# Optimization experiments

Hardware: AMD Instinct MI355X
Metric: run time of the kernel (lower is better)

The kernel has to match this reference:

```python
import math
import jax, jax.numpy as jnp
import numpy as np

N_ANGLES = 180  # len(thetas), thetas = k*pi/180 for k in 0..179
IMG_SIZE = 256
BATCH = 2


def setup_inputs() -> dict:
    key = jax.random.key(0)
    image = jax.random.normal(key, (BATCH, 1, IMG_SIZE, IMG_SIZE), dtype=jnp.float32)
    return {"image": image}


def _bilinear_gather(flat_img, yi, xi, S, dtype):
    # flat_img: (B, S*S); yi, xi: (A, S, S) int32 corner indices
    valid = (xi >= 0) & (xi < S) & (yi >= 0) & (yi < S)
    idx = jnp.clip(yi, 0, S - 1) * S + jnp.clip(xi, 0, S - 1)
    v = jnp.take(flat_img, idx.reshape(-1), axis=1).reshape((flat_img.shape[0],) + idx.shape)
    return v * valid.astype(dtype)  # zeros padding_mode


def reference(image):
    # Radon.forward with circle=False: pad image to diagonal size, rotate
    # sampling grid per angle, grid_sample (bilinear, align_corners=True,
    # padding_mode='zeros'), sum over rows -> sinogram (B, 1, S, n_angles).
    B, _, S0, _ = image.shape
    S = int(math.ceil(math.sqrt(2.0) * S0))  # padded size (363 for 256)
    pad_total = S - S0
    pb, pa = pad_total // 2, pad_total - pad_total // 2
    img = jnp.pad(image[:, 0], ((0, 0), (pb, pa), (pb, pa)))  # (B, S, S)

    thetas = jnp.arange(N_ANGLES, dtype=jnp.float32) * jnp.float32(np.pi / N_ANGLES)
    cos = jnp.cos(thetas)[:, None, None]  # (A,1,1)
    sin = jnp.sin(thetas)[:, None, None]

    # affine_grid(align_corners=True) base grid in [-1, 1]
    lin = jnp.linspace(-1.0, 1.0, S, dtype=jnp.float32)
    x = lin[None, None, :]  # width coord
    y = lin[None, :, None]  # height coord
    gx = cos * x + sin * y   # (A, S, S) sample x
    gy = -sin * x + cos * y  # (A, S, S) sample y

    # grid_sample align_corners=True pixel coordinates
    ix = (gx + 1.0) * 0.5 * (S - 1)
    iy = (gy + 1.0) * 0.5 * (S - 1)
    x0 = jnp.floor(ix)
    y0 = jnp.floor(iy)
    wx = ix - x0
    wy = iy - y0
    x0i = x0.astype(jnp.int32)
    y0i = y0.astype(jnp.int32)

    flat = img.reshape(B, S * S)
    dt = img.dtype
    v00 = _bilinear_gather(flat, y0i, x0i, S, dt)
    v01 = _bilinear_gather(flat, y0i, x0i + 1, S, dt)
    v10 = _bilinear_gather(flat, y0i + 1, x0i, S, dt)
    v11 = _bilinear_gather(flat, y0i + 1, x0i + 1, S, dt)

    samp = (v00 * (1 - wx) * (1 - wy) + v01 * wx * (1 - wy)
            + v10 * (1 - wx) * wy + v11 * wx * wy)  # (B, A, S, S)

    sino = samp.sum(axis=2)             # sum over rows -> (B, A, S)
    return sino.transpose(0, 2, 1)[:, None]  # (B, 1, S, A)
```

## Files before the change

kernel.cpp:

```cpp
#include <hip/hip_runtime.h>

#define N_ANGLES 180
#define IMG 256
#define SPAD 363
#define PB 53
#define BATCH 2
#define TOTAL (BATCH * N_ANGLES * SPAD)
#define RSPLIT 4

#define QB 6
#define QDIM (IMG + 2 * QB)
#define QELEMS (QDIM * QDIM)
#define NTAB (2 * BATCH)
#define COFF ((QB - PB) * (QDIM + 1))

__global__ __launch_bounds__(256) void prep_quad(const float* __restrict__ img,
                                                 float4* __restrict__ quad) {
    const int e = blockIdx.x * 256 + threadIdx.x;
    if (e >= NTAB * QELEMS) return;
    const int xq = e % QDIM;
    const int t2 = e / QDIM;
    const int yq = t2 % QDIM;
    const int tb = t2 / QDIM;
    const int b  = tb & (BATCH - 1);
    const int v  = tb >> 1;
    const int x = xq - QB, y = yq - QB;
    const float* ib = img + b * (IMG * IMG);
    auto val = [&](int yy, int xx) -> float {
        if ((unsigned)yy >= (unsigned)IMG || (unsigned)xx >= (unsigned)IMG) return 0.0f;
        return v ? ib[xx * IMG + yy]
                 : ib[yy * IMG + xx];
    };
    float4 q;
    q.x = val(y, x);     q.y = val(y, x + 1);
    q.z = val(y + 1, x); q.w = val(y + 1, x + 1);
    quad[e] = q;
}

__global__ __launch_bounds__(256) void radon_quad(const float4* __restrict__ quad,
                                                  float* __restrict__ out) {
    const int gid = blockIdx.x * 256 + threadIdx.x;
    const int o = gid >> 2;
    const int p = gid & 3;
    if (o >= TOTAL) return;

    const int t  = o % SPAD;
    const int ba = o / SPAD;
    const int a  = ba % N_ANGLES;
    const int b  = ba / N_ANGLES;

    const float theta = (float)a * 0.017453292519943295f;
    float s, c;
    sincosf(theta, &s, &c);

    const float d  = 2.0f / 362.0f;
    const float lt = fmaf((float)t, d, -1.0f);
    const float ct  = c * lt;
    const float mst = -s * lt;

    const bool useT = (s > fabsf(c));
    const float sA = useT ? c   : s;
    const float cA = useT ? mst : ct;
    const float sB = useT ? s   : c;
    const float cB = useT ? ct  : mst;
    const float4* __restrict__ qt = quad + ((useT ? BATCH : 0) + b) * QELEMS;

    const float fA = sA * 181.0f, gA = (cA + 1.0f) * 181.0f;
    const float fB = sB * 181.0f, gB = (cB + 1.0f) * 181.0f;
    const float v0A = fmaf(fA, -1.0f, gA), dvA = fA * d * 181.0f;
    const float v0B = fmaf(fB, -1.0f, gB), dvB = fB * d * 181.0f;
    const float stepA = fA * d;
    const float stepB = fB * d;

    float rlo = 0.0f, rhi = 362.0f;
    {
        const float lo = 51.0f, hi = 310.0f;
        if (fabsf(stepA) < 1e-5f) {
            if (v0A < lo || v0A > hi) { rlo = 363.0f; rhi = -1.0f; }
        } else {
            const float r0 = (lo - v0A) / stepA;
            const float r1 = (hi - v0A) / stepA;
            rlo = fmaxf(rlo, fminf(r0, r1));
            rhi = fminf(rhi, fmaxf(r0, r1));
        }
        if (fabsf(stepB) < 1e-5f) {
            if (v0B < lo || v0B > hi) { rlo = 363.0f; rhi = -1.0f; }
        } else {
            const float r0 = (lo - v0B) / stepB;
            const float r1 = (hi - v0B) / stepB;
            rlo = fmaxf(rlo, fminf(r0, r1));
            rhi = fminf(rhi, fmaxf(r0, r1));
        }
    }
    const int rmin = max(0,   (int)floorf(rlo));
    const int rmax = min(362, (int)ceilf(rhi));

    float acc = 0.0f;
#pragma unroll 2
    for (int r = rmin + ((p - rmin) & 3); r <= rmax; r += RSPLIT) {
        const float rf = (float)r;
        const float ix = fmaf(rf, stepA, v0A);
        const float iy = fmaf(rf, stepB, v0B);
        const float wx = ix - floorf(ix);
        const float wy = iy - floorf(iy);
        const int   xi = (int)ix;
        const int   yi = (int)iy;
        const float4 q = qt[yi * QDIM + xi + COFF];
        const float omwx = 1.0f - wx;
        const float omwy = 1.0f - wy;
        const float top = fmaf(q.y, wx, q.x * omwx);
        const float bot = fmaf(q.w, wx, q.z * omwx);
        acc = fmaf(bot, wy, fmaf(top, omwy, acc));
    }

    acc += __shfl_xor(acc, 1);
    acc += __shfl_xor(acc, 2);

    if (p == 0) {
        out[(b * SPAD + t) * N_ANGLES + a] = acc;
    }
}


__global__ __launch_bounds__(256) void transpose_kernel(const float* __restrict__ img,
                                                        float* __restrict__ imgT) {
    __shared__ float tile[32][33];
    const int b  = blockIdx.z;
    const int tx = blockIdx.x * 32;
    const int ty = blockIdx.y * 32;
    const int lx = threadIdx.x & 31;
    const int l8 = threadIdx.x >> 5;
    const float* ib = img  + b * IMG * IMG;
    float*       ob = imgT + b * IMG * IMG;
#pragma unroll
    for (int i = 0; i < 4; ++i) {
        const int ly = l8 + i * 8;
        tile[ly][lx] = ib[(ty + ly) * IMG + tx + lx];
    }
    __syncthreads();
#pragma unroll
    for (int i = 0; i < 4; ++i) {
        const int ly = l8 + i * 8;
        ob[(tx + ly) * IMG + ty + lx] = tile[lx][ly];
    }
}

#define SAMPLE(r, CHECKED)                                                     \
    {                                                                          \
        const float lr  = fmaf((float)(r), d, -1.0f);                          \
        const float ix  = fmaf(fA, lr, gA);                                    \
        const float iy  = fmaf(fB, lr, gB);                                    \
        const float wx  = ix - floorf(ix);                                     \
        const float wy  = iy - floorf(iy);                                     \
        const int   xi  = (int)ix;                                             \
        const int   yi  = (int)iy;                                             \
        float v00, v01, v10, v11;                                              \
        if (CHECKED) {                                                         \
            const int xA = xi - PB, yA = yi - PB;                              \
            const bool vx0 = (unsigned)xA       < (unsigned)IMG;               \
            const bool vx1 = (unsigned)(xA + 1) < (unsigned)IMG;               \
            const bool vy0 = (unsigned)yA       < (unsigned)IMG;               \
            const bool vy1 = (unsigned)(yA + 1) < (unsigned)IMG;               \
            const float* rp = base + yA * IMG + xA;                            \
            v00 = (vx0 && vy0) ? rp[0]       : 0.0f;                           \
            v01 = (vx1 && vy0) ? rp[1]       : 0.0f;                           \
            v10 = (vx0 && vy1) ? rp[IMG]     : 0.0f;                           \
            v11 = (vx1 && vy1) ? rp[IMG + 1] : 0.0f;                           \
        } else {                                                               \
            const float* rp = base + (yi * IMG + xi - (PB * IMG + PB));        \
            v00 = rp[0]; v01 = rp[1]; v10 = rp[IMG]; v11 = rp[IMG + 1];        \
        }                                                                      \
        const float omwx = 1.0f - wx;                                          \
        const float omwy = 1.0f - wy;                                          \
        const float top  = fmaf(v01, wx, v00 * omwx);                          \
        const float bot  = fmaf(v11, wx, v10 * omwx);                          \
        acc = fmaf(bot, wy, fmaf(top, omwy, acc));                             \
    }

template <bool HAVE_T>
__global__ __launch_bounds__(256) void radon_kernel(const float* __restrict__ img,
                                                    const float* __restrict__ imgT,
                                                    float* __restrict__ out) {
    const int gid = blockIdx.x * 256 + threadIdx.x;
    const int o = gid >> 1;
    const int p = gid & 1;
    if (o >= TOTAL) return;

    const int t  = o % SPAD;
    const int ba = o / SPAD;
    const int a  = ba % N_ANGLES;
    const int b  = ba / N_ANGLES;

    const float theta = (float)a * 0.017453292519943295f;
    float s, c;
    sincosf(theta, &s, &c);

    const float d  = 2.0f / 362.0f;
    const float lt = fmaf((float)t, d, -1.0f);
    const float ct  = c * lt;
    const float mst = -s * lt;

    const bool useT = HAVE_T && (s > fabsf(c));
    const float sA = useT ? c   : s;
    const float cA = useT ? mst : ct;
    const float sB = useT ? s   : c;
    const float cB = useT ? ct  : mst;
    const float* __restrict__ base = (useT ? imgT : img) + b * (IMG * IMG);

    const float fA = sA * 181.0f;
    const float gA = (cA + 1.0f) * 181.0f;
    const float fB = sB * 181.0f;
    const float gB = (cB + 1.0f) * 181.0f;

    const float v0A = fmaf(fA, -1.0f, gA), dvA = fA * d;
    const float v0B = fmaf(fB, -1.0f, gB), dvB = fB * d;

    auto clip = [](float v0, float dv, float lo, float hi, float& rlo, float& rhi) {
        if (fabsf(dv) < 1e-5f) {
            if (v0 < lo || v0 > hi) { rlo = 363.0f; rhi = -1.0f; }
        } else {
            const float r0 = (lo - v0) / dv;
            const float r1 = (hi - v0) / dv;
            rlo = fmaxf(rlo, fminf(r0, r1));
            rhi = fminf(rhi, fmaxf(r0, r1));
        }
    };

    float rloA = 0.0f, rhiA = 362.0f;
    clip(v0A, dvA, 51.0f, 310.0f, rloA, rhiA);
    clip(v0B, dvB, 51.0f, 310.0f, rloA, rhiA);
    const int rmin = max(0,   (int)floorf(rloA));
    const int rmax = min(362, (int)ceilf(rhiA));

    float rloI = (float)rmin, rhiI = (float)rmax;
    clip(v0A, dvA, 54.0f, 307.0f, rloI, rhiI);
    clip(v0B, dvB, 54.0f, 307.0f, rloI, rhiI);
    int rin_lo = (int)ceilf(rloI);
    int rin_hi = (int)floorf(rhiI);
    if (rin_lo < rmin) rin_lo = rmin;
    if (rin_hi > rmax) rin_hi = rmax;
    if (rin_lo > rin_hi) { rin_lo = rmax + 1; rin_hi = rmax; }

    float acc = 0.0f;
    for (int r = rmin + ((p - rmin) & 1); r < rin_lo; r += 2)
        SAMPLE(r, true);
#pragma unroll 2
    for (int r = rin_lo + ((p - rin_lo) & 1); r <= rin_hi; r += 2)
        SAMPLE(r, false);
    for (int r = rin_hi + 1 + ((p - rin_hi - 1) & 1); r <= rmax; r += 2)
        SAMPLE(r, true);

    acc += __shfl_xor(acc, 1);

    if (p == 0) {
        out[(b * SPAD + t) * N_ANGLES + a] = acc;
    }
}

extern "C" void kernel_launch(void* const* d_in, const int* in_sizes, int n_in,
                              void* d_out, int out_size, void* d_ws, size_t ws_size,
                              hipStream_t stream) {
    const float* img = (const float*)d_in[0];
    float* out = (float*)d_out;

    const size_t needQ = (size_t)NTAB * QELEMS * sizeof(float4);
    if (ws_size >= needQ) {
        float4* quad = (float4*)d_ws;
        prep_quad<<<(NTAB * QELEMS + 255) / 256, 256, 0, stream>>>(img, quad);
        const int threads = TOTAL * RSPLIT;
        radon_quad<<<(threads + 255) / 256, 256, 0, stream>>>(quad, out);
    } else if (ws_size >= (size_t)(BATCH * IMG * IMG * sizeof(float))) {
        float* imgT = (float*)d_ws;
        transpose_kernel<<<dim3(8, 8, 2), 256, 0, stream>>>(img, imgT);
        const int threads = TOTAL * 2;
        radon_kernel<true><<<(threads + 255) / 256, 256, 0, stream>>>(img, imgT, out);
    } else {
        const int threads = TOTAL * 2;
        radon_kernel<false><<<(threads + 255) / 256, 256, 0, stream>>>(img, nullptr, out);
    }
}
```

Before: 95.68 us.

## Reorder angle-to-block mapping and swizzle blocks across XCDs, dual accumulators

Remaps blocks so that consecutive blocks cycle across 8 groups (XCD-style swizzle). Angles are also reordered so that angles sharing the transposed table and similar access patterns land in contiguous ranges, which should give better L2 locality per die and less wavefront divergence on useT. The ray loop is manually unrolled into two independent accumulators to break the FMA dependency chain. The grid is padded to 2048 blocks with early exit for unused ones.

```diff
diff --git a/kernel.cpp b/kernel.cpp
--- a/kernel.cpp
+++ b/kernel.cpp
@@ -7,6 +7,8 @@
 #define BATCH 2
 #define TOTAL (BATCH * N_ANGLES * SPAD)
 #define RSPLIT 4
+#define NBLK ((TOTAL + 63) / 64)
+#define NPAD 2048
 
 #define QB 6
 #define QDIM (IMG + 2 * QB)
@@ -37,17 +39,38 @@
     quad[e] = q;
 }
 
+#define SAMP(r, A)                                                             \
+    {                                                                          \
+        const float rf = (float)(r);                                           \
+        const float ix = fmaf(rf, stepA, v0A);                                 \
+        const float iy = fmaf(rf, stepB, v0B);                                 \
+        const float wx = ix - floorf(ix);         \
+        const float wy = iy - floorf(iy);                                      \
+        const int   xi = (int)ix;                \
+        const int   yi = (int)iy;                                              \
+        const float4 q = qt[yi * QDIM + xi + COFF];                            \
+        const float omwx = 1.0f - wx;                                          \
+        const float omwy = 1.0f - wy;                                          \
+        const float top = fmaf(q.y, wx, q.x * omwx);                           \
+        const float bot = fmaf(q.w, wx, q.z * omwx);                           \
+        A = fmaf(bot, wy, fmaf(top, omwy, A));                                 \
+    }
+
 __global__ __launch_bounds__(256) void radon_quad(const float4* __restrict__ quad,
                                                   float* __restrict__ out) {
-    const int gid = blockIdx.x * 256 + threadIdx.x;
-    const int o = gid >> 2;
-    const int p = gid & 3;
+    const int L  = blockIdx.x;
+    const int ob = (L & 7) * (NPAD / 8) + (L >> 3);
+    if (ob >= NBLK) return;
+    const int o = ob * 64 + (threadIdx.x >> 2);
+    const int p = threadIdx.x & 3;
     if (o >= TOTAL) return;
 
-    const int t  = o % SPAD;
-    const int ba = o / SPAD;
-    const int a  = ba % N_ANGLES;
-    const int b  = ba / N_ANGLES;
+    const int t = o % SPAD;
+    const int g = o / SPAD;
+    const int j = g % 180;
+    const int b = g / 180;
+    const int a = j + (j < 46 ? 0 : (j < 91 ? 89 : -45));
+    const bool useT = (j >= 91);
 
     const float theta = (float)a * 0.017453292519943295f;
     float s, c;
@@ -58,7 +81,6 @@
     const float ct  = c * lt;
     const float mst = -s * lt;
 
-    const bool useT = (s > fabsf(c));
     const float sA = useT ? c   : s;
     const float cA = useT ? mst : ct;
     const float sB = useT ? s   : c;
@@ -67,10 +89,8 @@
 
     const float fA = sA * 181.0f, gA = (cA + 1.0f) * 181.0f;
     const float fB = sB * 181.0f, gB = (cB + 1.0f) * 181.0f;
-    const float v0A = fmaf(fA, -1.0f, gA), dvA = fA * d * 181.0f;
-    const float v0B = fmaf(fB, -1.0f, gB), dvB = fB * d * 181.0f;
-    const float stepA = fA * d;
-    const float stepB = fB * d;
+    const float v0A = fmaf(fA, -1.0f, gA), stepA = fA * d;
+    const float v0B = fmaf(fB, -1.0f, gB), stepB = fB * d;
 
     float rlo = 0.0f, rhi = 362.0f;
     {
@@ -95,23 +115,15 @@
     const int rmin = max(0,   (int)floorf(rlo));
     const int rmax = min(362, (int)ceilf(rhi));
 
-    float acc = 0.0f;
+    float acc0 = 0.0f, acc1 = 0.0f;
+    int r = rmin + ((p - rmin) & 3);
 #pragma unroll 2
-    for (int r = rmin + ((p - rmin) & 3); r <= rmax; r += RSPLIT) {
-        const float rf = (float)r;
-        const float ix = fmaf(rf, stepA, v0A);
-        const float iy = fmaf(rf, stepB, v0B);
-        const float wx = ix - floorf(ix);
-        const float wy = iy - floorf(iy);
-        const int   xi = (int)ix;
-        const int   yi = (int)iy;
-        const float4 q = qt[yi * QDIM + xi + COFF];
-        const float omwx = 1.0f - wx;
-        const float omwy = 1.0f - wy;
-        const float top = fmaf(q.y, wx, q.x * omwx);
-        const float bot = fmaf(q.w, wx, q.z * omwx);
-        acc = fmaf(bot, wy, fmaf(top, omwy, acc));
-    }
+    for (; r + 4 <= rmax; r += 8) {
+        SAMP(r, acc0);
+        SAMP(r + 4, acc1);
+    }
+    if (r <= rmax) SAMP(r, acc0);
+    float acc = acc0 + acc1;
 
     acc += __shfl_xor(acc, 1);
     acc += __shfl_xor(acc, 2);
@@ -267,8 +279,7 @@
     if (ws_size >= needQ) {
         float4* quad = (float4*)d_ws;
         prep_quad<<<(NTAB * QELEMS + 255) / 256, 256, 0, stream>>>(img, quad);
-        const int threads = TOTAL * RSPLIT;
-        radon_quad<<<(threads + 255) / 256, 256, 0, stream>>>(quad, out);
+        radon_quad<<<NPAD, 256, 0, stream>>>(quad, out);
     } else if (ws_size >= (size_t)(BATCH * IMG * IMG * sizeof(float))) {
         float* imgT = (float*)d_ws;
         transpose_kernel<<<dim3(8, 8, 2), 256, 0, stream>>>(img, imgT);
```

Result: no change. 95.27 us (-0.4%).
